# Performance work log

Measured on AMD Instinct MI355X. Metric: run time of the kernel, lower is better.

Reference implementation:

```python
import jax, jax.numpy as jnp
import numpy as np

EPS = 1e-6


def _sparse_conv(feats, nbr, mask, W):
    # feats: [N, C], nbr: [N, K] int, mask: [N, K] bool, W: [K, C, Cout]
    g = jnp.where(mask[..., None], feats[nbr], 0.0)  # gather: [N, K, C]
    return jnp.einsum('nkc,kcd->nd', g, W)           # GEMM + scatter-free accumulate


def _layernorm(x, gamma, beta):
    mu = jnp.mean(x, axis=-1, keepdims=True)
    var = jnp.mean(jnp.square(x - mu), axis=-1, keepdims=True)
    return (x - mu) * jax.lax.rsqrt(var + EPS) * gamma + beta


def setup_inputs() -> dict:
    key = jax.random.key(0)
    ks = jax.random.split(key, 6)
    N, K, C = 100000, 9, 256
    w_scale = 1.0 / np.sqrt(K * C)  # fan-in init so activations stay O(1)
    feats = jax.random.normal(ks[0], (N, C), dtype=jnp.float32)
    W1 = jax.random.normal(ks[1], (K, C, C), dtype=jnp.float32) * w_scale
    W2 = jax.random.normal(ks[2], (K, C, C), dtype=jnp.float32) * w_scale
    gamma1 = jnp.ones((C,), dtype=jnp.float32)
    beta1 = jnp.zeros((C,), dtype=jnp.float32)
    gamma2 = jnp.ones((C,), dtype=jnp.float32)
    beta2 = jnp.zeros((C,), dtype=jnp.float32)
    neighbor_idx = jax.random.randint(ks[3], (N, K), 0, N, dtype=jnp.int32)
    neighbor_mask = jax.random.bernoulli(ks[4], 0.7, (N, K))
    return {"feats": feats, "W1": W1, "gamma1": gamma1, "beta1": beta1,
            "W2": W2, "gamma2": gamma2, "beta2": beta2,
            "neighbor_idx": neighbor_idx, "neighbor_mask": neighbor_mask}


def reference(feats, W1, gamma1, beta1, W2, gamma2, beta2, neighbor_idx, neighbor_mask):
    residual = feats
    out = _sparse_conv(feats, neighbor_idx, neighbor_mask, W1)   # conv1 (stride 1)
    out = _layernorm(out, gamma1, beta1)                          # norm1
    out = jax.nn.gelu(out, approximate=False)                     # act
    out = _sparse_conv(out, neighbor_idx, neighbor_mask, W2)      # conv2
    out = _layernorm(out, gamma2, beta2)                          # norm2
    out = out + residual                                          # downsample is None
    out = jax.nn.gelu(out, approximate=False)
    return out
```

## Files before the change

kernel.cpp:

```cpp
#include <hip/hip_runtime.h>
#include <hip/hip_bf16.h>
#include <math.h>

#define C 256
#define K 9
#define BM 64
#define NKSTEP 72
#define HSTEPS 18

typedef __attribute__((ext_vector_type(8))) short bf16x8;
typedef __attribute__((ext_vector_type(4))) float f32x4;

__device__ __forceinline__ unsigned short f2bf(float f) {
    unsigned int u = __float_as_uint(f);
    unsigned int r = (u + 0x7fffu + ((u >> 16) & 1u)) >> 16;
    return (unsigned short)r;
}

__device__ __forceinline__ float gelu_exact(float x) {
    return 0.5f * x * (1.0f + erff(x * 0.70710678118654752f));
}

__global__ void detect_mask_kernel(const unsigned char* __restrict__ mb, int nbytes,
                                   unsigned int* __restrict__ cnt) {
    unsigned int l0 = 0, l12 = 0;
    for (int i = blockIdx.x * blockDim.x + threadIdx.x; i < nbytes;
         i += blockDim.x * gridDim.x) {
        unsigned char v = mb[i];
        if (v) {
            int r = i & 3;
            if (r == 0) l0 = 1;
            else if (r < 3) l12 = 1;
        }
    }
    unsigned long long b0 = __ballot(l0 != 0);
    unsigned long long b1 = __ballot(l12 != 0);
    if ((threadIdx.x & 63) == 0) {
        if (b0) atomicOr(&cnt[0], 1u);
        if (b1) atomicOr(&cnt[1], 1u);
    }
}

__global__ void pack_w(const float* __restrict__ W, unsigned short* __restrict__ Wp) {
    int id = blockIdx.x * blockDim.x + threadIdx.x;
    if (id >= NKSTEP * 16 * 64) return;
    int lane = id & 63;
    int ctg  = (id >> 6) & 15;
    int kkg  = id >> 10;
    int tap  = kkg >> 3;
    int c    = (kkg & 7) * 32 + ((lane >> 4) << 3);
    int d    = ctg * 16 + (lane & 15);
    const float* src = W + ((size_t)tap * C + c) * C + d;
    unsigned int w[4];
    #pragma unroll
    for (int i = 0; i < 4; ++i) {
        unsigned short lo = f2bf(src[(size_t)(2 * i) * C]);
        unsigned short hi = f2bf(src[(size_t)(2 * i + 1) * C]);
        w[i] = (unsigned int)lo | ((unsigned int)hi << 16);
    }
    uint4 v = {w[0], w[1], w[2], w[3]};
    *(uint4*)(Wp + (size_t)id * 8) = v;
}

template<int PHASE>
__global__ __launch_bounds__(256, 2)
void conv_mfma(const float* __restrict__ srcf,
               const char* __restrict__ gbase,
               const unsigned short* __restrict__ Wp,
               const float* __restrict__ gamma, const float* __restrict__ beta,
               const int* __restrict__ nbr, const void* __restrict__ mask,
               const unsigned int* __restrict__ mflags,
               const float* __restrict__ resid,
               void* __restrict__ dst,
               int N)
{
    __shared__ __align__(16) unsigned short Abuf[2][BM * 128];
    __shared__ unsigned int offs[K][BM];
    __shared__ float part[BM][8];

    const int tid  = threadIdx.x;
    const int lane = tid & 63;
    const int wv   = tid >> 6;
    const int n0   = blockIdx.x * BM;

    const bool mbool = (mflags[0] != 0u) && (mflags[1] != 0u);
    const unsigned char* mask8  = (const unsigned char*)mask;
    const unsigned int*  mask32 = (const unsigned int*)mask;
    for (int e = tid; e < K * BM; e += 256) {
        int tap = e >> 6;
        int r   = e & (BM - 1);
        int row = n0 + r;
        unsigned int off = (PHASE == 1) ? 0xFFFFFFFFu : 0u;
        if (row < N) {
            size_t ei = (size_t)row * K + tap;
            bool mv = mbool ? (mask8[ei] != 0) : (mask32[ei] != 0u);
            if (mv) off = (PHASE == 1) ? (unsigned int)nbr[ei] * 1024u
                                       : 512u + (unsigned int)nbr[ei] * 512u;
        }
        offs[tap][r] = off;
    }
    __syncthreads();

    f32x4 acc[4][4];
    #pragma unroll
    for (int rt = 0; rt < 4; ++rt)
        #pragma unroll
        for (int ct = 0; ct < 4; ++ct)
            acc[rt][ct] = (f32x4){0.f, 0.f, 0.f, 0.f};

    float4 pre[8];
    bool pmask = true;

    auto issue1 = [&](int s) {
        int tap = s >> 1; int h = (s & 1) * 512;
        int r = tid >> 2, q = tid & 3;
        unsigned int off = offs[tap][r];
        pmask = (off == 0xFFFFFFFFu);
        if (!pmask) {
            const char* base = (const char*)srcf + off + h + q * 128;
            #pragma unroll
            for (int i = 0; i < 4; ++i) {
                pre[i * 2]     = *(const float4*)(base + i * 32);
                pre[i * 2 + 1] = *(const float4*)(base + i * 32 + 16);
            }
        }
    };
    auto write1 = [&](int b) {
        int r = tid >> 2, q = tid & 3;
        #pragma unroll
        for (int i = 0; i < 4; ++i) {
            int c16 = q * 4 + i;
            uint4 v;
            if (pmask) {
                v = (uint4){0u, 0u, 0u, 0u};
            } else {
                float4 a = pre[i * 2], bvec = pre[i * 2 + 1];
                v.x = (unsigned int)f2bf(a.x) | ((unsigned int)f2bf(a.y) << 16);
                v.y = (unsigned int)f2bf(a.z) | ((unsigned int)f2bf(a.w) << 16);
                v.z = (unsigned int)f2bf(bvec.x) | ((unsigned int)f2bf(bvec.y) << 16);
                v.w = (unsigned int)f2bf(bvec.z) | ((unsigned int)f2bf(bvec.w) << 16);
            }
            *(uint4*)(&Abuf[b][r * 128 + ((c16 ^ (r & 7)) * 8)]) = v;
        }
    };

    auto stage2 = [&](int s, int b) {
        int tap = s >> 1; int h = (s & 1) * 256;
        #pragma unroll
        for (int i = wv * 4; i < wv * 4 + 4; ++i) {
            int r = i * 4 + (lane >> 4);
            int c16s = ((lane & 15) ^ (r & 7)) * 16;
            const char* g = gbase + offs[tap][r] + h + c16s;
            __builtin_amdgcn_global_load_lds((const __attribute__((address_space(1))) void*)g,
                (__attribute__((address_space(3))) void*)(&Abuf[b][i * 512]), 16, 0, 0);
        }
    };

    auto compute = [&](int s, int p) {
        #pragma unroll
        for (int kk = 0; kk < 4; ++kk) {
            int kkg = s * 4 + kk;
            bf16x8 bfr[4], afr[4];
            #pragma unroll
            for (int ct = 0; ct < 4; ++ct)
                bfr[ct] = *(const bf16x8*)(Wp + (((size_t)kkg * 16 + (wv * 4 + ct)) * 64 + lane) * 8);
            #pragma unroll
            for (int rt = 0; rt < 4; ++rt) {
                int r = rt * 16 + (lane & 15);
                int c16 = kk * 4 + (lane >> 4);
                afr[rt] = *(const bf16x8*)(&Abuf[p][r * 128 + ((c16 ^ (r & 7)) * 8)]);
            }
            #pragma unroll
            for (int rt = 0; rt < 4; ++rt)
                #pragma unroll
                for (int ct = 0; ct < 4; ++ct)
                    acc[rt][ct] = __builtin_amdgcn_mfma_f32_16x16x32_bf16(afr[rt], bfr[ct], acc[rt][ct], 0, 0, 0);
        }
    };

    int p = 0;
    if (PHASE == 1) {
        issue1(0);
        write1(0);
        __syncthreads();
        for (int s = 0; s < HSTEPS; ++s) {
            if (s + 1 < HSTEPS) issue1(s + 1);
            compute(s, p);
            __syncthreads();
            if (s + 1 < HSTEPS) {
                write1(p ^ 1);
                __syncthreads();
            }
            p ^= 1;
        }
    } else {
        stage2(0, 0);
        __syncthreads();
        for (int s = 0; s < HSTEPS; ++s) {
            if (s + 1 < HSTEPS) stage2(s + 1, p ^ 1);
            compute(s, p);
            __syncthreads();
            p ^= 1;
        }
    }

    #pragma unroll
    for (int rt = 0; rt < 4; ++rt) {
        #pragma unroll
        for (int jj = 0; jj < 4; ++jj) {
            float p1 = 0.f, p2 = 0.f;
            #pragma unroll
            for (int ct = 0; ct < 4; ++ct) {
                float v = acc[rt][ct][jj];
                p1 += v; p2 += v * v;
            }
            #pragma unroll
            for (int off = 1; off < 16; off <<= 1) {
                p1 += __shfl_xor(p1, off, 64);
                p2 += __shfl_xor(p2, off, 64);
            }
            if ((lane & 15) == 0) {
                int row = rt * 16 + (lane >> 4) * 4 + jj;
                part[row][wv * 2]     = p1;
                part[row][wv * 2 + 1] = p2;
            }
        }
    }
    __syncthreads();

    float gm[4], bt[4];
    #pragma unroll
    for (int ct = 0; ct < 4; ++ct) {
        int col = wv * 64 + ct * 16 + (lane & 15);
        gm[ct] = gamma[col]; bt[ct] = beta[col];
    }
    const float inv_c = 1.0f / 256.0f;
    #pragma unroll
    for (int rt = 0; rt < 4; ++rt) {
        #pragma unroll
        for (int jj = 0; jj < 4; ++jj) {
            int row = rt * 16 + (lane >> 4) * 4 + jj;
            float t1 = part[row][0] + part[row][2] + part[row][4] + part[row][6];
            float t2 = part[row][1] + part[row][3] + part[row][5] + part[row][7];
            float mu  = t1 * inv_c;
            float var = t2 * inv_c - mu * mu;
            float rs  = rsqrtf(var + 1e-6f);
            int grow = n0 + row;
            if (grow < N) {
                #pragma unroll
                for (int ct = 0; ct < 4; ++ct) {
                    int col = wv * 64 + ct * 16 + (lane & 15);
                    float x = (acc[rt][ct][jj] - mu) * rs * gm[ct] + bt[ct];
                    if (PHASE == 2) x += resid[(size_t)grow * C + col];
                    float o = gelu_exact(x);
                    if (PHASE == 1) ((unsigned short*)dst)[(size_t)grow * C + col] = f2bf(o);
                    else            ((float*)dst)[(size_t)grow * C + col] = o;
                }
            }
        }
    }
}

extern "C" void kernel_launch(void* const* d_in, const int* in_sizes, int n_in,
                              void* d_out, int out_size, void* d_ws, size_t ws_size,
                              hipStream_t stream) {
    const float* feats = (const float*)d_in[0];
    const float* W1    = (const float*)d_in[1];
    const float* g1    = (const float*)d_in[2];
    const float* b1    = (const float*)d_in[3];
    const float* W2    = (const float*)d_in[4];
    const float* g2    = (const float*)d_in[5];
    const float* b2    = (const float*)d_in[6];
    const int*   nbr   = (const int*)d_in[7];
    const void*  mask  = (const void*)d_in[8];

    const int N = in_sizes[0] / C;

    char* ws = (char*)d_ws;
    unsigned short* h1  = (unsigned short*)(ws + 512);
    size_t h1_bytes = (size_t)N * C * 2;
    unsigned short* Wp1 = (unsigned short*)(ws + 512 + h1_bytes);
    size_t wp_bytes = (size_t)NKSTEP * 16 * 64 * 8 * 2;
    unsigned short* Wp2 = (unsigned short*)(ws + 512 + h1_bytes + wp_bytes);
    unsigned int* mflags = (unsigned int*)(ws + 512 + h1_bytes + 2 * wp_bytes);

    hipMemsetAsync(ws, 0, 512, stream);
    hipMemsetAsync(mflags, 0, 2 * sizeof(unsigned int), stream);
    detect_mask_kernel<<<256, 256, 0, stream>>>((const unsigned char*)mask, N * K, mflags);
    pack_w<<<(NKSTEP * 16 * 64 + 255) / 256, 256, 0, stream>>>(W1, Wp1);
    pack_w<<<(NKSTEP * 16 * 64 + 255) / 256, 256, 0, stream>>>(W2, Wp2);

    const int grid = (N + BM - 1) / BM;
    conv_mfma<1><<<grid, 256, 0, stream>>>(feats, nullptr, Wp1, g1, b1, nbr, mask, mflags,
                                           nullptr, (void*)h1, N);
    conv_mfma<2><<<grid, 256, 0, stream>>>(nullptr, ws, Wp2, g2, b2, nbr, mask, mflags,
                                           feats, d_out, N);
}
```

Baseline: 669.5 us.

## Pre-convert feats to bf16 and use triple-buffered async LDS gather in both convs

Adds a kernel that converts the fp32 input features to bf16 into a zero-padded scratch area inside the output buffer. This lets conv1 use the same direct global-to-LDS gather path that conv2 already uses, in place of register loads followed by conversion. The LDS pipeline goes from two to three buffers with a prefetch distance of two, using explicit vmcnt waits and raw barriers, and the occupancy hint rises to three blocks per SM. The cost is an extra pass over feats plus heavier LDS use. Correctness also depends on conv2 reading the residual from fp32 feats while overwriting d_out, which held the bf16 copy.

```diff
diff --git a/kernel.cpp b/kernel.cpp
--- a/kernel.cpp
+++ b/kernel.cpp
@@ -7,6 +7,7 @@
 #define BM 64
 #define NKSTEP 72
 #define HSTEPS 18
+#define NBUF 3
 
 typedef __attribute__((ext_vector_type(8))) short bf16x8;
 typedef __attribute__((ext_vector_type(4))) float f32x4;
@@ -39,6 +40,19 @@
         if (b0) atomicOr(&cnt[0], 1u);
         if (b1) atomicOr(&cnt[1], 1u);
     }
+}
+
+__global__ void convert_feats(const float* __restrict__ in, unsigned short* __restrict__ out, int n8) {
+    int i = blockIdx.x * blockDim.x + threadIdx.x;
+    if (i >= n8) return;
+    const float4* p = (const float4*)(in + (size_t)i * 8);
+    float4 a = p[0], b = p[1];
+    uint4 v;
+    v.x = (unsigned int)f2bf(a.x) | ((unsigned int)f2bf(a.y) << 16);
+    v.y = (unsigned int)f2bf(a.z) | ((unsigned int)f2bf(a.w) << 16);
+    v.z = (unsigned int)f2bf(b.x) | ((unsigned int)f2bf(b.y) << 16);
+    v.w = (unsigned int)f2bf(b.z) | ((unsigned int)f2bf(b.w) << 16);
+    *(uint4*)(out + (size_t)i * 8) = v;
 }
 
 __global__ void pack_w(const float* __restrict__ W, unsigned short* __restrict__ Wp) {
@@ -63,9 +77,8 @@
 }
 
 template<int PHASE>
-__global__ __launch_bounds__(256, 2)
-void conv_mfma(const float* __restrict__ srcf,
-               const char* __restrict__ gbase,
+__global__ __launch_bounds__(256, 3)
+void conv_mfma(const char* __restrict__ gbase,
                const unsigned short* __restrict__ Wp,
                const float* __restrict__ gamma, const float* __restrict__ beta,
                const int* __restrict__ nbr, const void* __restrict__ mask,
@@ -74,7 +87,7 @@
                void* __restrict__ dst,
                int N)
 {
-    __shared__ __align__(16) unsigned short Abuf[2][BM * 128];
+    __shared__ __align__(16) unsigned short Abuf[NBUF][BM * 128];
     __shared__ unsigned int offs[K][BM];
     __shared__ float part[BM][8];
 
@@ -90,16 +103,14 @@
         int tap = e >> 6;
         int r   = e & (BM - 1);
         int row = n0 + r;
-        unsigned int off = (PHASE == 1) ? 0xFFFFFFFFu : 0u;
+        unsigned int off = 0u;
         if (row < N) {
             size_t ei = (size_t)row * K + tap;
             bool mv = mbool ? (mask8[ei] != 0) : (mask32[ei] != 0u);
-            if (mv) off = (PHASE == 1) ? (unsigned int)nbr[ei] * 1024u
-                                       : 512u + (unsigned int)nbr[ei] * 512u;
+            if (mv) off = 512u + (unsigned int)nbr[ei] * 512u;
         }
         offs[tap][r] = off;
     }
-    __syncthreads();
 
     f32x4 acc[4][4];
     #pragma unroll
@@ -108,46 +119,13 @@
         for (int ct = 0; ct < 4; ++ct)
             acc[rt][ct] = (f32x4){0.f, 0.f, 0.f, 0.f};
 
-    float4 pre[8];
-    bool pmask = true;
-
-    auto issue1 = [&](int s) {
-        int tap = s >> 1; int h = (s & 1) * 512;
-        int r = tid >> 2, q = tid & 3;
-        unsigned int off = offs[tap][r];
-        pmask = (off == 0xFFFFFFFFu);
-        if (!pmask) {
-            const char* base = (const char*)srcf + off + h + q * 128;
-            #pragma unroll
-            for (int i = 0; i < 4; ++i) {
-                pre[i * 2]     = *(const float4*)(base + i * 32);
-                pre[i * 2 + 1] = *(const float4*)(base + i * 32 + 16);
-            }
-        }
-    };
-    auto write1 = [&](int b) {
-        int r = tid >> 2, q = tid & 3;
-        #pragma unroll
-        for (int i = 0; i < 4; ++i) {
-            int c16 = q * 4 + i;
-            uint4 v;
-            if (pmask) {
-                v = (uint4){0u, 0u, 0u, 0u};
-            } else {
-                float4 a = pre[i * 2], bvec = pre[i * 2 + 1];
-                v.x = (unsigned int)f2bf(a.x) | ((unsigned int)f2bf(a.y) << 16);
-                v.y = (unsigned int)f2bf(a.z) | ((unsigned int)f2bf(a.w) << 16);
-                v.z = (unsigned int)f2bf(bvec.x) | ((unsigned int)f2bf(bvec.y) << 16);
-                v.w = (unsigned int)f2bf(bvec.z) | ((unsigned int)f2bf(bvec.w) << 16);
-            }
-            *(uint4*)(&Abuf[b][r * 128 + ((c16 ^ (r & 7)) * 8)]) = v;
-        }
-    };
-
-    auto stage2 = [&](int s, int b) {
-        int tap = s >> 1; int h = (s & 1) * 256;
-        #pragma unroll
-        for (int i = wv * 4; i < wv * 4 + 4; ++i) {
+    __syncthreads();
+
+    auto stage = [&](int s, int b) {
+        int tap = s >> 1, h = (s & 1) * 256;
+        #pragma unroll
+        for (int ii = 0; ii < 4; ++ii) {
+            int i = wv * 4 + ii;
             int r = i * 4 + (lane >> 4);
             int c16s = ((lane & 15) ^ (r & 7)) * 16;
             const char* g = gbase + offs[tap][r] + h + c16s;
@@ -156,7 +134,7 @@
         }
     };
 
-    auto compute = [&](int s, int p) {
+    auto compute = [&](int s, int b) {
         #pragma unroll
         for (int kk = 0; kk < 4; ++kk) {
             int kkg = s * 4 + kk;
@@ -168,7 +146,7 @@
             for (int rt = 0; rt < 4; ++rt) {
                 int r = rt * 16 + (lane & 15);
                 int c16 = kk * 4 + (lane >> 4);
-                afr[rt] = *(const bf16x8*)(&Abuf[p][r * 128 + ((c16 ^ (r & 7)) * 8)]);
+                afr[rt] = *(const bf16x8*)(&Abuf[b][r * 128 + ((c16 ^ (r & 7)) * 8)]);
             }
             #pragma unroll
             for (int rt = 0; rt < 4; ++rt)
@@ -178,30 +156,23 @@
         }
     };
 
-    int p = 0;
-    if (PHASE == 1) {
-        issue1(0);
-        write1(0);
-        __syncthreads();
-        for (int s = 0; s < HSTEPS; ++s) {
-            if (s + 1 < HSTEPS) issue1(s + 1);
-            compute(s, p);
-            __syncthreads();
-            if (s + 1 < HSTEPS) {
-                write1(p ^ 1);
-                __syncthreads();
-            }
-            p ^= 1;
-        }
-    } else {
-        stage2(0, 0);
-        __syncthreads();
-        for (int s = 0; s < HSTEPS; ++s) {
-            if (s + 1 < HSTEPS) stage2(s + 1, p ^ 1);
-            compute(s, p);
-            __syncthreads();
-            p ^= 1;
-        }
+    stage(0, 0);
+    stage(1, 1);
+
+    int bs = 0;
+    for (int s = 0; s < HSTEPS; ++s) {
+        if (s < HSTEPS - 1) { asm volatile("s_waitcnt vmcnt(4)" ::: "memory"); }
+        else                { asm volatile("s_waitcnt vmcnt(0)" ::: "memory"); }
+        __builtin_amdgcn_sched_barrier(0);
+        __builtin_amdgcn_s_barrier();
+        __builtin_amdgcn_sched_barrier(0);
+        if (s + 2 < HSTEPS) {
+            int bn = bs + 2 >= NBUF ? bs + 2 - NBUF : bs + 2;
+            stage(s + 2, bn);
+        }
+        compute(s, bs);
+        __builtin_amdgcn_sched_barrier(0);
+        bs = (bs + 1 == NBUF) ? 0 : bs + 1;
     }
 
     #pragma unroll
@@ -278,21 +249,26 @@
 
     char* ws = (char*)d_ws;
     unsigned short* h1  = (unsigned short*)(ws + 512);
-    size_t h1_bytes = (size_t)N * C * 2;
-    unsigned short* Wp1 = (unsigned short*)(ws + 512 + h1_bytes);
-    size_t wp_bytes = (size_t)NKSTEP * 16 * 64 * 8 * 2;
-    unsigned short* Wp2 = (unsigned short*)(ws + 512 + h1_bytes + wp_bytes);
-    unsigned int* mflags = (unsigned int*)(ws + 512 + h1_bytes + 2 * wp_bytes);
+    size_t h1_bytes = 512 + (size_t)N * C * 2;
+    size_t wp_bytes = (size_t)NKSTEP * 16 * 64 * 16;
+    unsigned short* Wp1 = (unsigned short*)(ws + h1_bytes);
+    unsigned short* Wp2 = (unsigned short*)(ws + h1_bytes + wp_bytes);
+    unsigned int* mflags = (unsigned int*)(ws + h1_bytes + 2 * wp_bytes);
+
+    char* fzone = (char*)d_out;
+    unsigned short* featsb = (unsigned short*)(fzone + 512);
 
     hipMemsetAsync(ws, 0, 512, stream);
+    hipMemsetAsync(fzone, 0, 512, stream);
     hipMemsetAsync(mflags, 0, 2 * sizeof(unsigned int), stream);
     detect_mask_kernel<<<256, 256, 0, stream>>>((const unsigned char*)mask, N * K, mflags);
+    convert_feats<<<(N * C / 8 + 255) / 256, 256, 0, stream>>>(feats, featsb, N * C / 8);
     pack_w<<<(NKSTEP * 16 * 64 + 255) / 256, 256, 0, stream>>>(W1, Wp1);
     pack_w<<<(NKSTEP * 16 * 64 + 255) / 256, 256, 0, stream>>>(W2, Wp2);
 
     const int grid = (N + BM - 1) / BM;
-    conv_mfma<1><<<grid, 256, 0, stream>>>(feats, nullptr, Wp1, g1, b1, nbr, mask, mflags,
+    conv_mfma<1><<<grid, 256, 0, stream>>>(fzone, Wp1, g1, b1, nbr, mask, mflags,
                                            nullptr, (void*)h1, N);
-    conv_mfma<2><<<grid, 256, 0, stream>>>(nullptr, ws, Wp2, g2, b2, nbr, mask, mflags,
+    conv_mfma<2><<<grid, 256, 0, stream>>>(ws, Wp2, g2, b2, nbr, mask, mflags,
                                            feats, d_out, N);
 }
```

After: 627.6 us. 1.07x faster.
